# Kernel optimization log

Measured on AMD Instinct MI355X. Metric: run time of the kernel, lower is better.

The kernel has to match this reference:

```python
import jax, jax.numpy as jnp
import numpy as np

N, HID, EDGE_DIM, E = 512, 16, 8, 8192
H4 = HID * 4


def _mlp(x, params):
    W0, b0, W1, b1, W2, b2, W3, b3 = params
    h = jax.nn.relu(x @ W0 + b0)
    h = jax.nn.relu(h @ W1 + b1)
    h = jax.nn.relu(h @ W2 + b2)
    return h @ W3 + b3


def setup_inputs() -> dict:
    key = jax.random.key(0)
    ks = jax.random.split(key, 16)
    rng = np.random.default_rng(0)
    flat = rng.choice(N * N, size=E, replace=False)  # unique edges -> add == set
    edge_index = jnp.asarray(np.stack([flat // N, flat % N]), dtype=jnp.int32)

    def lin(k, fan_in, fan_out):
        kw, kb = jax.random.split(k)
        s = 1.0 / np.sqrt(fan_in)
        return (jax.random.uniform(kw, (fan_in, fan_out), jnp.float32, -s, s),
                jax.random.uniform(kb, (fan_out,), jnp.float32, -s, s))

    W0, b0 = lin(ks[0], EDGE_DIM, H4)
    W1, b1 = lin(ks[1], H4, H4)
    W2, b2 = lin(ks[2], H4, H4)
    W3, b3 = lin(ks[3], H4, HID * HID)
    V0, c0 = lin(ks[4], HID, H4)
    V1, c1 = lin(ks[5], H4, H4)
    V2, c2 = lin(ks[6], H4, H4)
    V3, c3 = lin(ks[7], H4, HID)
    L, Lb = lin(ks[8], HID, HID)

    return {
        'mtr': jax.random.normal(ks[9], (N, N, HID), jnp.float32),
        'edge_attr': jax.random.normal(ks[10], (E, EDGE_DIM), jnp.float32),
        'edge_index': edge_index,
        'W0': W0, 'b0': b0, 'W1': W1, 'b1': b1, 'W2': W2, 'b2': b2, 'W3': W3, 'b3': b3,
        'V0': V0, 'c0': c0, 'V1': V1, 'c1': c1, 'V2': V2, 'c2': c2, 'V3': V3, 'c3': c3,
        'L': L, 'Lb': Lb,
    }


def reference(mtr, edge_attr, edge_index,
              W0, b0, W1, b1, W2, b2, W3, b3,
              V0, c0, V1, c1, V2, c2, V3, c3,
              L, Lb):
    n, hid = mtr.shape[0], mtr.shape[2]
    src, dst = edge_index[0], edge_index[1]
    # per-edge hid x hid matrices (edge_fc)
    F = _mlp(edge_attr, (W0, b0, W1, b1, W2, b2, W3, b3)).reshape(-1, hid, hid)
    # sparse form of einsum('ijc,jkct->ikt', mtr, fmtr): gather src column,
    # per-edge matmul, scatter-add into dst column (edges unique -> == dense set)
    msg = jnp.einsum('iec,ect->iet', mtr[:, src, :], F)          # [n, E, hid]
    mtr1 = jax.ops.segment_sum(msg.transpose(1, 0, 2), dst, num_segments=n)  # [k, i, t]
    mtr1 = mtr1.transpose(1, 0, 2)                                # [i, k, t]
    idx = jnp.arange(n)
    mtr1 = mtr1.at[idx, idx, :].set(0.0)
    mtr1 = mtr1 / hid
    trans = mtr1.transpose(1, 0, 2) @ L + Lb                      # linear(mtr1^T)
    return mtr + _mlp(mtr1 + trans, (V0, c0, V1, c1, V2, c2, V3, c3))
```

## Files before the change

### kernel.cpp

```cpp
#include <hip/hip_runtime.h>
#include <hip/hip_bf16.h>

#define NN 512
#define EE 8192

#define OFF_F     0u
#define OFF_MTR1  2097152u
#define OFF_W     6291456u
#define WR_W0   0
#define WR_B0   512
#define WR_W1   576
#define WR_B1   4672
#define WR_W2   4736
#define WR_B2   8832
#define WR_W3   8896
#define WR_B3   25280
#define WR_V0T  25536
#define WR_C0   26560
#define WR_V1   26624
#define WR_C1   30720
#define WR_V2   30784
#define WR_C2   34880
#define WR_V3   34944
#define WR_C3   35968
#define WR_L    35984
#define WR_LB   36240
#define W_TOTAL 36256
#define OFF_OFFS    (OFF_W + W_TOTAL)
#define OFF_SORTED  (OFF_OFFS + 513)
#define OFF_FLAG    (OFF_SORTED + EE)
#define OFF_MTRT    6336420u
#define OFF_OFFSP   8433572u
#define OFF_PACKP   8434085u
#define OFF_FPACK   8442792u
#define OFF_VPACK   9491496u
#define WS_NEED_BYTES  ((size_t)(OFF_MTRT  + 2097152u) * 4u)
#define WS_FULL2_BYTES ((size_t)(OFF_VPACK + 5632u) * 4u)

#define VP0OFF 0
#define VP1OFF 2048
#define VP2OFF 6144
#define VP3OFF 10240

#define XSTR 72
#define RSTR 20

typedef __attribute__((ext_vector_type(8))) short bf16x8;
typedef __attribute__((ext_vector_type(4))) float f32x4;

__device__ __forceinline__ float bflo(unsigned u){ return __uint_as_float(u << 16); }
__device__ __forceinline__ float bfhi(unsigned u){ return __uint_as_float(u & 0xffff0000u); }
__device__ __forceinline__ unsigned short f2bf(float f){
  __hip_bfloat16 h = __float2bfloat16(f);
  union { __hip_bfloat16 hh; unsigned short ss; } u;
  u.hh = h; return u.ss;
}
__device__ __forceinline__ unsigned pack2(float a, float b){
  return (unsigned)f2bf(a) | ((unsigned)f2bf(b) << 16);
}
__device__ __forceinline__ float cvt(float v){ return v; }
__device__ __forceinline__ float cvt(__hip_bfloat16 v){ return __bfloat162float(v); }

__device__ __forceinline__ void load16f(const void* base, size_t eoff, int f32, float m[16]) {
  if (f32) {
    const float4* p = (const float4*)((const float*)base + eoff);
    float4 a = p[0], b = p[1], c = p[2], d = p[3];
    m[0]=a.x; m[1]=a.y; m[2]=a.z; m[3]=a.w;
    m[4]=b.x; m[5]=b.y; m[6]=b.z; m[7]=b.w;
    m[8]=c.x; m[9]=c.y; m[10]=c.z; m[11]=c.w;
    m[12]=d.x; m[13]=d.y; m[14]=d.z; m[15]=d.w;
  } else {
    const uint4* p = (const uint4*)((const __hip_bfloat16*)base + eoff);
    uint4 u0 = p[0], u1 = p[1];
    m[0]=bflo(u0.x);  m[1]=bfhi(u0.x);  m[2]=bflo(u0.y);  m[3]=bfhi(u0.y);
    m[4]=bflo(u0.z);  m[5]=bfhi(u0.z);  m[6]=bflo(u0.w);  m[7]=bfhi(u0.w);
    m[8]=bflo(u1.x);  m[9]=bfhi(u1.x);  m[10]=bflo(u1.y); m[11]=bfhi(u1.y);
    m[12]=bflo(u1.z); m[13]=bfhi(u1.z); m[14]=bflo(u1.w); m[15]=bfhi(u1.w);
  }
}

__device__ __forceinline__ float ldelem(const void* p, int idx, int f32) {
  return f32 ? ((const float*)p)[idx]
             : __bfloat162float(((const __hip_bfloat16*)p)[idx]);
}

__device__ __forceinline__ int detect_f32_local(const unsigned short* mtr_u16, float* red) {
  int tid = threadIdx.x;
  float m = 0.f;
  for (int t = tid; t < 4096; t += 512) {
    float v = __uint_as_float(((unsigned)mtr_u16[t]) << 16);
    if (v != v) m = 3e38f;
    else m = fmaxf(m, fabsf(v));
  }
  red[tid] = m;
  __syncthreads();
  for (int s = 256; s > 0; s >>= 1) {
    if (tid < s) red[tid] = fmaxf(red[tid], red[tid + s]);
    __syncthreads();
  }
  float mx = red[0];
  __syncthreads();
  return (mx > 1e6f) ? 1 : 0;
}

template <typename T>
__device__ void edge_body(const T* __restrict__ ea,
                          const T* __restrict__ W0, const T* __restrict__ b0,
                          const T* __restrict__ W1, const T* __restrict__ b1,
                          const T* __restrict__ W2, const T* __restrict__ b2,
                          const T* __restrict__ W3, const T* __restrict__ b3,
                          int e, int eg, int lane,
                          float (*shA)[64], float (*shB)[64],
                          unsigned short* __restrict__ Fpack)
{
  float x[8];
  #pragma unroll
  for (int c = 0; c < 8; c++) x[c] = cvt(ea[(size_t)e * 8 + c]);

  float s = cvt(b0[lane]);
  #pragma unroll
  for (int c = 0; c < 8; c++) s += x[c] * cvt(W0[c * 64 + lane]);
  shA[eg][lane] = fmaxf(s, 0.f);
  __syncthreads();

  s = cvt(b1[lane]);
  #pragma unroll
  for (int c = 0; c < 64; c++) s += shA[eg][c] * cvt(W1[c * 64 + lane]);
  shB[eg][lane] = fmaxf(s, 0.f);
  __syncthreads();

  s = cvt(b2[lane]);
  #pragma unroll
  for (int c = 0; c < 64; c++) s += shB[eg][c] * cvt(W2[c * 64 + lane]);
  shA[eg][lane] = fmaxf(s, 0.f);
  __syncthreads();

  int quad = lane >> 4, tt = lane & 15;
  #pragma unroll
  for (int r = 0; r < 4; r++) {
    int o = r * 64 + lane;
    float t = cvt(b3[o]);
    #pragma unroll
    for (int c = 0; c < 64; c++) t += shA[eg][c] * cvt(W3[c * 256 + o]);
    int cc = r * 4 + quad;
    Fpack[(size_t)e * 256 + (cc >> 3) * 128 + tt * 8 + (cc & 7)] = f2bf(t);
  }
}

__global__ __launch_bounds__(512) void prep_all(
  const void* __restrict__ mtr, const void* __restrict__ ea, const int* __restrict__ ei,
  const void* __restrict__ W0, const void* __restrict__ b0,
  const void* __restrict__ W1, const void* __restrict__ b1,
  const void* __restrict__ W2, const void* __restrict__ b2,
  const void* __restrict__ W3, const void* __restrict__ b3,
  const void* __restrict__ V0, const void* __restrict__ c0,
  const void* __restrict__ V1, const void* __restrict__ c1,
  const void* __restrict__ V2, const void* __restrict__ c2,
  const void* __restrict__ V3, const void* __restrict__ c3,
  const void* __restrict__ L,  const void* __restrict__ Lb,
  int* __restrict__ flag, float* __restrict__ w, unsigned short* __restrict__ VP,
  int* __restrict__ offsP, unsigned* __restrict__ packP,
  unsigned short* __restrict__ Fpack, __hip_bfloat16* __restrict__ mtrT)
{
  __shared__ __attribute__((aligned(16))) char smem_raw[8192];
  int tid = threadIdx.x;
  int bid = blockIdx.x;
  const int f32 = detect_f32_local((const unsigned short*)mtr, (float*)smem_raw);

  if (bid == 0) {
    int* cnt  = (int*)smem_raw;
    int* pcs  = cnt + 512;
    int* curP = pcs + 512;
    cnt[tid] = 0;
    if (tid == 0) flag[0] = f32;
    __syncthreads();
    for (int e = tid; e < EE; e += 512) atomicAdd(&cnt[ei[EE + e]], 1);
    __syncthreads();
    int myc = cnt[tid];
    int myp = (myc + 1) & ~1;
    pcs[tid] = myp;
    __syncthreads();
    for (int off = 1; off < 512; off <<= 1) {
      int b = (tid >= off) ? pcs[tid - off] : 0;
      __syncthreads();
      pcs[tid] += b;
      __syncthreads();
    }
    int excP = pcs[tid] - myp;
    offsP[tid] = excP;
    if (tid == 511) offsP[512] = pcs[511];
    curP[tid] = excP;
    if (myc & 1) packP[excP + myc] = EE;
    __syncthreads();
    for (int e = tid; e < EE; e += 512) {
      int d = ei[EE + e];
      int s = ei[e];
      packP[atomicAdd(&curP[d], 1)] = (unsigned)e | ((unsigned)s << 14);
    }
    unsigned* fz = (unsigned*)(Fpack + (size_t)EE * 256);
    for (int i2 = tid; i2 < 128; i2 += 512) fz[i2] = 0u;
  } else if (bid < 33) {
    int g = (bid - 1) * 512 + tid;
    const int stride = 32 * 512;
    auto cv = [&](const void* p, int off, int n){
      for (int i = g; i < n; i += stride) w[off + i] = ldelem(p, i, f32);
    };
    cv(W0, WR_W0, 512);  cv(b0, WR_B0, 64);
    cv(W1, WR_W1, 4096); cv(b1, WR_B1, 64);
    cv(W2, WR_W2, 4096); cv(b2, WR_B2, 64);
    cv(W3, WR_W3, 16384);cv(b3, WR_B3, 256);
    for (int idx = g; idx < 1024; idx += stride) {
      int j = idx >> 4, t = idx & 15;
      w[WR_V0T + idx] = ldelem(V0, t * 64 + j, f32);
    }
    cv(c0, WR_C0, 64);
    cv(V1, WR_V1, 4096); cv(c1, WR_C1, 64);
    cv(V2, WR_V2, 4096); cv(c2, WR_C2, 64);
    cv(V3, WR_V3, 1024); cv(c3, WR_C3, 16);
    cv(L,  WR_L,  256);  cv(Lb, WR_LB, 16);
  } else if (bid < 37) {
    int g = (bid - 33) * 512 + tid;
    const int stride = 4 * 512;
    for (int idx = g; idx < 2048; idx += stride) {
      int j = idx & 7, lp = (idx >> 3) & 63, nt = idx >> 9;
      int nn = lp & 15, qq = lp >> 4;
      int kk = qq * 8 + j;
      float v = (kk < 16) ? ldelem(V0, kk * 64 + nt * 16 + nn, f32) : 0.f;
      VP[VP0OFF + idx] = f2bf(v);
    }
    for (int idx = g; idx < 4096; idx += stride) {
      int j = idx & 7, lp = (idx >> 3) & 63, tile = idx >> 9;
      int nn = lp & 15, qq = lp >> 4;
      int kc = tile >> 2, nt = tile & 3;
      int kk = kc * 32 + qq * 8 + j;
      VP[VP1OFF + idx] = f2bf(ldelem(V1, kk * 64 + nt * 16 + nn, f32));
      VP[VP2OFF + idx] = f2bf(ldelem(V2, kk * 64 + nt * 16 + nn, f32));
    }
    for (int idx = g; idx < 1024; idx += stride) {
      int j = idx & 7, lp = (idx >> 3) & 63, kc = idx >> 9;
      int nn = lp & 15, qq = lp >> 4;
      int kk = kc * 32 + qq * 8 + j;
      VP[VP3OFF + idx] = f2bf(ldelem(V3, kk * 16 + nn, f32));
    }
  } else if (bid < 549) {
    int s = bid - 37;
    int i = tid;
    float m[16];
    load16f(mtr, (size_t)i * 8192 + (size_t)s * 16, f32, m);
    unsigned pw[8];
    #pragma unroll
    for (int q = 0; q < 8; q++) pw[q] = pack2(m[2*q], m[2*q+1]);
    uint4* op = (uint4*)(mtrT + (size_t)s * 8192 + (size_t)i * 16);
    op[0] = make_uint4(pw[0], pw[1], pw[2], pw[3]);
    op[1] = make_uint4(pw[4], pw[5], pw[6], pw[7]);
  } else {
    int eg = tid >> 6, lane = tid & 63;
    int e = (bid - 549) * 8 + eg;
    float (*shA)[64] = (float(*)[64])smem_raw;
    float (*shB)[64] = (float(*)[64])(smem_raw + 2048);
    if (f32)
      edge_body<float>((const float*)ea,
        (const float*)W0, (const float*)b0, (const float*)W1, (const float*)b1,
        (const float*)W2, (const float*)b2, (const float*)W3, (const float*)b3,
        e, eg, lane, shA, shB, Fpack);
    else
      edge_body<__hip_bfloat16>((const __hip_bfloat16*)ea,
        (const __hip_bfloat16*)W0, (const __hip_bfloat16*)b0,
        (const __hip_bfloat16*)W1, (const __hip_bfloat16*)b1,
        (const __hip_bfloat16*)W2, (const __hip_bfloat16*)b2,
        (const __hip_bfloat16*)W3, (const __hip_bfloat16*)b3,
        e, eg, lane, shA, shB, Fpack);
  }
}

__global__ __launch_bounds__(256) void message_mfma2(
  const __hip_bfloat16* __restrict__ mtrT,
  const unsigned short* __restrict__ Fpack,
  const int* __restrict__ offsP, const unsigned* __restrict__ packP,
  float* __restrict__ mtr1T)
{
  int k = blockIdx.x;
  int tid = threadIdx.x;
  int wave = tid >> 6, lane = tid & 63;
  int n = lane & 15, quad = lane >> 4;
  int qh = quad >> 1, qq = quad & 1;
  int ibase = blockIdx.y * 256 + wave * 64;
  int j0 = offsP[k], j1 = offsP[k + 1];

  f32x4 acc[4];
  #pragma unroll
  for (int mt = 0; mt < 4; mt++) acc[mt] = (f32x4){0.f, 0.f, 0.f, 0.f};

  bf16x8 bfrag;
  bf16x8 af0, af1, af2, af3;
  auto loadfr = [&](int j) {
    unsigned p1 = __builtin_amdgcn_readfirstlane(packP[j]);
    unsigned p2 = __builtin_amdgcn_readfirstlane(packP[j + 1]);
    unsigned pv = qh ? p2 : p1;
    int es = (int)(pv & 0x3FFFu);
    int ss = (int)(pv >> 14);
    bfrag = *(const bf16x8*)(Fpack + (size_t)es * 256 + (qq * 16 + n) * 8);
    const __hip_bfloat16* ab = mtrT + (size_t)ss * 8192 + qq * 8;
    af0 = *(const bf16x8*)(ab + (size_t)(ibase + 0 * 16 + n) * 16);
    af1 = *(const bf16x8*)(ab + (size_t)(ibase + 1 * 16 + n) * 16);
    af2 = *(const bf16x8*)(ab + (size_t)(ibase + 2 * 16 + n) * 16);
    af3 = *(const bf16x8*)(ab + (size_t)(ibase + 3 * 16 + n) * 16);
  };
  if (j0 < j1) loadfr(j0);
  for (int j = j0; j < j1; j += 2) {
    bf16x8 bc = bfrag, a0 = af0, a1 = af1, a2 = af2, a3 = af3;
    if (j + 2 < j1) loadfr(j + 2);
    acc[0] = __builtin_amdgcn_mfma_f32_16x16x32_bf16(a0, bc, acc[0], 0, 0, 0);
    acc[1] = __builtin_amdgcn_mfma_f32_16x16x32_bf16(a1, bc, acc[1], 0, 0, 0);
    acc[2] = __builtin_amdgcn_mfma_f32_16x16x32_bf16(a2, bc, acc[2], 0, 0, 0);
    acc[3] = __builtin_amdgcn_mfma_f32_16x16x32_bf16(a3, bc, acc[3], 0, 0, 0);
  }

  float* obase = mtr1T + (size_t)k * 8192;
  #pragma unroll
  for (int mt = 0; mt < 4; mt++) {
    int irow = ibase + mt * 16 + quad * 4;
    #pragma unroll
    for (int reg = 0; reg < 4; reg++)
      obase[(size_t)(irow + reg) * 16 + n] = acc[mt][reg];
  }
}

__global__ __launch_bounds__(256, 4) void final_mfma(
  const void* __restrict__ mtr, const float* __restrict__ w,
  const float* __restrict__ mtr1T, const int* __restrict__ flag,
  const unsigned short* __restrict__ VP, void* __restrict__ out)
{
  const int f32 = flag[0];
  __shared__ __attribute__((aligned(16))) unsigned short XB[256 * XSTR];
  int tid = threadIdx.x;
  int ti = blockIdx.x >> 5, tk = blockIdx.x & 31;
  int r = tid >> 4, c = tid & 15;
  int i = ti * 16 + r, k = tk * 16 + c;
  float scale = (i == k) ? 0.f : 0.0625f;

  float y[16];
  {
    float a[16], b[16];
    const float4* pa = (const float4*)(mtr1T + (size_t)k * 8192 + (size_t)i * 16);
    const float4* pb = (const float4*)(mtr1T + (size_t)i * 8192 + (size_t)k * 16);
    #pragma unroll
    for (int q4 = 0; q4 < 4; q4++) {
      float4 va = pa[q4], vb = pb[q4];
      a[q4*4+0]=va.x*scale; a[q4*4+1]=va.y*scale; a[q4*4+2]=va.z*scale; a[q4*4+3]=va.w*scale;
      b[q4*4+0]=vb.x*scale; b[q4*4+1]=vb.y*scale; b[q4*4+2]=vb.z*scale; b[q4*4+3]=vb.w*scale;
    }
    const float* Lf  = w + WR_L;
    const float* Lbf = w + WR_LB;
    #pragma unroll
    for (int t = 0; t < 16; t++) y[t] = a[t] + Lbf[t];
    #pragma unroll
    for (int cc = 0; cc < 16; cc++) {
      #pragma unroll
      for (int t = 0; t < 16; t++) y[t] += b[cc] * Lf[cc * 16 + t];
    }
  }
  {
    uint4* row = (uint4*)(XB + tid * XSTR);
    row[0] = make_uint4(pack2(y[0],y[1]),  pack2(y[2],y[3]),
                        pack2(y[4],y[5]),  pack2(y[6],y[7]));
    row[1] = make_uint4(pack2(y[8],y[9]),  pack2(y[10],y[11]),
                        pack2(y[12],y[13]),pack2(y[14],y[15]));
    row[2] = make_uint4(0,0,0,0);
    row[3] = make_uint4(0,0,0,0);
  }

  int wave = tid >> 6, lane = tid & 63;
  int m15 = lane & 15, q = lane >> 4;
  int mtb = wave * 4;

  {
    bf16x8 af[4];
    #pragma unroll
    for (int t4 = 0; t4 < 4; t4++)
      af[t4] = *(const bf16x8*)(XB + ((mtb + t4) * 16 + m15) * XSTR + q * 8);
    #pragma unroll
    for (int nt = 0; nt < 4; nt++) {
      bf16x8 bf_ = *(const bf16x8*)(VP + VP0OFF + nt * 512 + (q * 16 + m15) * 8);
      float bias = w[WR_C0 + nt * 16 + m15];
      #pragma unroll
      for (int t4 = 0; t4 < 4; t4++) {
        f32x4 acc = (f32x4){0.f,0.f,0.f,0.f};
        acc = __builtin_amdgcn_mfma_f32_16x16x32_bf16(af[t4], bf_, acc, 0, 0, 0);
        int pbase = (mtb + t4) * 16 + q * 4;
        #pragma unroll
        for (int reg = 0; reg < 4; reg++)
          XB[(pbase + reg) * XSTR + nt * 16 + m15] = f2bf(fmaxf(acc[reg] + bias, 0.f));
      }
    }
  }
  #pragma unroll
  for (int layer = 0; layer < 2; layer++) {
    int vpo  = layer ? VP2OFF : VP1OFF;
    int wrc  = layer ? WR_C2  : WR_C1;
    bf16x8 af[8];
    #pragma unroll
    for (int t4 = 0; t4 < 4; t4++) {
      #pragma unroll
      for (int kc = 0; kc < 2; kc++)
        af[t4*2+kc] = *(const bf16x8*)(XB + ((mtb + t4) * 16 + m15) * XSTR + kc * 32 + q * 8);
    }
    #pragma unroll
    for (int nt = 0; nt < 4; nt++) {
      bf16x8 b0 = *(const bf16x8*)(VP + vpo + (0 * 4 + nt) * 512 + (q * 16 + m15) * 8);
      bf16x8 b1 = *(const bf16x8*)(VP + vpo + (1 * 4 + nt) * 512 + (q * 16 + m15) * 8);
      float bias = w[wrc + nt * 16 + m15];
      #pragma unroll
      for (int t4 = 0; t4 < 4; t4++) {
        f32x4 acc = (f32x4){0.f,0.f,0.f,0.f};
        acc = __builtin_amdgcn_mfma_f32_16x16x32_bf16(af[t4*2+0], b0, acc, 0, 0, 0);
        acc = __builtin_amdgcn_mfma_f32_16x16x32_bf16(af[t4*2+1], b1, acc, 0, 0, 0);
        int pbase = (mtb + t4) * 16 + q * 4;
        #pragma unroll
        for (int reg = 0; reg < 4; reg++)
          XB[(pbase + reg) * XSTR + nt * 16 + m15] = f2bf(fmaxf(acc[reg] + bias, 0.f));
      }
    }
  }
  f32x4 acc4[4];
  float bias4;
  {
    bf16x8 af[8];
    #pragma unroll
    for (int t4 = 0; t4 < 4; t4++) {
      #pragma unroll
      for (int kc = 0; kc < 2; kc++)
        af[t4*2+kc] = *(const bf16x8*)(XB + ((mtb + t4) * 16 + m15) * XSTR + kc * 32 + q * 8);
    }
    bf16x8 b0 = *(const bf16x8*)(VP + VP3OFF + 0 * 512 + (q * 16 + m15) * 8);
    bf16x8 b1 = *(const bf16x8*)(VP + VP3OFF + 1 * 512 + (q * 16 + m15) * 8);
    bias4 = w[WR_C3 + m15];
    #pragma unroll
    for (int t4 = 0; t4 < 4; t4++) {
      f32x4 acc = (f32x4){0.f,0.f,0.f,0.f};
      acc = __builtin_amdgcn_mfma_f32_16x16x32_bf16(af[t4*2+0], b0, acc, 0, 0, 0);
      acc = __builtin_amdgcn_mfma_f32_16x16x32_bf16(af[t4*2+1], b1, acc, 0, 0, 0);
      acc4[t4] = acc;
    }
  }
  __syncthreads();
  float* RRB = (float*)XB;
  #pragma unroll
  for (int t4 = 0; t4 < 4; t4++) {
    int pbase = (mtb + t4) * 16 + q * 4;
    #pragma unroll
    for (int reg = 0; reg < 4; reg++)
      RRB[(pbase + reg) * RSTR + m15] = acc4[t4][reg] + bias4;
  }
  float rr[16];
  {
    const float4* rp = (const float4*)(RRB + tid * RSTR);
    float4 v0 = rp[0], v1 = rp[1], v2 = rp[2], v3 = rp[3];
    rr[0]=v0.x; rr[1]=v0.y; rr[2]=v0.z; rr[3]=v0.w;
    rr[4]=v1.x; rr[5]=v1.y; rr[6]=v1.z; rr[7]=v1.w;
    rr[8]=v2.x; rr[9]=v2.y; rr[10]=v2.z; rr[11]=v2.w;
    rr[12]=v3.x; rr[13]=v3.y; rr[14]=v3.z; rr[15]=v3.w;
  }
  size_t base = (size_t)i * 8192 + (size_t)k * 16;
  float mv[16];
  load16f(mtr, base, f32, mv);
  if (f32) {
    float4* op = (float4*)((float*)out + base);
    op[0] = make_float4(mv[0]+rr[0],  mv[1]+rr[1],  mv[2]+rr[2],  mv[3]+rr[3]);
    op[1] = make_float4(mv[4]+rr[4],  mv[5]+rr[5],  mv[6]+rr[6],  mv[7]+rr[7]);
    op[2] = make_float4(mv[8]+rr[8],  mv[9]+rr[9],  mv[10]+rr[10],mv[11]+rr[11]);
    op[3] = make_float4(mv[12]+rr[12],mv[13]+rr[13],mv[14]+rr[14],mv[15]+rr[15]);
  } else {
    unsigned pw[8];
    #pragma unroll
    for (int q2 = 0; q2 < 8; q2++)
      pw[q2] = pack2(mv[2*q2] + rr[2*q2], mv[2*q2+1] + rr[2*q2+1]);
    uint4* op = (uint4*)((__hip_bfloat16*)out + base);
    op[0] = make_uint4(pw[0], pw[1], pw[2], pw[3]);
    op[1] = make_uint4(pw[4], pw[5], pw[6], pw[7]);
  }
}

__global__ void prep_weights(
  const void* __restrict__ W0, const void* __restrict__ b0,
  const void* __restrict__ W1, const void* __restrict__ b1,
  const void* __restrict__ W2, const void* __restrict__ b2,
  const void* __restrict__ W3, const void* __restrict__ b3,
  const void* __restrict__ V0, const void* __restrict__ c0,
  const void* __restrict__ V1, const void* __restrict__ c1,
  const void* __restrict__ V2, const void* __restrict__ c2,
  const void* __restrict__ V3, const void* __restrict__ c3,
  const void* __restrict__ L,  const void* __restrict__ Lb,
  const unsigned short* __restrict__ mtr_u16,
  int* __restrict__ flag, float* __restrict__ w)
{
  __shared__ float mx[256];
  int tid = threadIdx.x;
  float m = 0.f;
  for (int t = tid; t < 4096; t += 256) {
    float v = __uint_as_float(((unsigned)mtr_u16[t]) << 16);
    if (v != v) m = 3e38f;
    else m = fmaxf(m, fabsf(v));
  }
  mx[tid] = m;
  __syncthreads();
  for (int s = 128; s > 0; s >>= 1) {
    if (tid < s) mx[tid] = fmaxf(mx[tid], mx[tid + s]);
    __syncthreads();
  }
  const int f32 = (mx[0] > 1e6f) ? 1 : 0;
  if (blockIdx.x == 0 && tid == 0) flag[0] = f32;

  int g = blockIdx.x * blockDim.x + tid;
  int stride = gridDim.x * blockDim.x;
  auto cv = [&](const void* p, int off, int n){
    for (int i = g; i < n; i += stride) w[off + i] = ldelem(p, i, f32);
  };
  cv(W0, WR_W0, 512);  cv(b0, WR_B0, 64);
  cv(W1, WR_W1, 4096); cv(b1, WR_B1, 64);
  cv(W2, WR_W2, 4096); cv(b2, WR_B2, 64);
  cv(W3, WR_W3, 16384);cv(b3, WR_B3, 256);
  for (int idx = g; idx < 1024; idx += stride) {
    int j = idx >> 4, t = idx & 15;
    w[WR_V0T + idx] = ldelem(V0, t * 64 + j, f32);
  }
  cv(c0, WR_C0, 64);
  cv(V1, WR_V1, 4096); cv(c1, WR_C1, 64);
  cv(V2, WR_V2, 4096); cv(c2, WR_C2, 64);
  cv(V3, WR_V3, 1024); cv(c3, WR_C3, 16);
  cv(L,  WR_L,  256);  cv(Lb, WR_LB, 16);
}

__global__ void build_bins_basic(const int* __restrict__ ei,
                                 int* __restrict__ offs, int* __restrict__ sorted)
{
  __shared__ int cnt[512];
  __shared__ int cur[512];
  int tid = threadIdx.x;
  cnt[tid] = 0;
  __syncthreads();
  for (int e = tid; e < EE; e += 512) atomicAdd(&cnt[ei[EE + e]], 1);
  __syncthreads();
  int myc = cnt[tid];
  for (int off = 1; off < 512; off <<= 1) {
    int add = (tid >= off) ? cnt[tid - off] : 0;
    __syncthreads();
    cnt[tid] += add;
    __syncthreads();
  }
  int excl = cnt[tid] - myc;
  offs[tid] = excl;
  if (tid == 511) offs[512] = cnt[511];
  cur[tid] = excl;
  __syncthreads();
  for (int e = tid; e < EE; e += 512) {
    int d = ei[EE + e];
    sorted[atomicAdd(&cur[d], 1)] = e;
  }
}

__global__ __launch_bounds__(256) void edge_mlp_fb(
  const void* __restrict__ ea, const float* __restrict__ w,
  const int* __restrict__ flag, float* __restrict__ Fws)
{
  const int f32 = flag[0];
  const float* W0f = w + WR_W0; const float* b0f = w + WR_B0;
  const float* W1f = w + WR_W1; const float* b1f = w + WR_B1;
  const float* W2f = w + WR_W2; const float* b2f = w + WR_B2;
  const float* W3f = w + WR_W3; const float* b3f = w + WR_B3;
  int tid = threadIdx.x;
  int eg = tid >> 6, lane = tid & 63;
  int e = blockIdx.x * 4 + eg;
  __shared__ float shA[4][64];
  __shared__ float shB[4][64];
  float x[8];
  #pragma unroll
  for (int c = 0; c < 8; c++) x[c] = ldelem(ea, e * 8 + c, f32);
  float s = b0f[lane];
  #pragma unroll
  for (int c = 0; c < 8; c++) s += x[c] * W0f[c * 64 + lane];
  shA[eg][lane] = fmaxf(s, 0.f);
  __syncthreads();
  s = b1f[lane];
  #pragma unroll
  for (int c = 0; c < 64; c++) s += shA[eg][c] * W1f[c * 64 + lane];
  shB[eg][lane] = fmaxf(s, 0.f);
  __syncthreads();
  s = b2f[lane];
  #pragma unroll
  for (int c = 0; c < 64; c++) s += shB[eg][c] * W2f[c * 64 + lane];
  shA[eg][lane] = fmaxf(s, 0.f);
  __syncthreads();
  #pragma unroll
  for (int r2 = 0; r2 < 4; r2++) {
    int o = r2 * 64 + lane;
    float t = b3f[o];
    #pragma unroll
    for (int c = 0; c < 64; c++) t += shA[eg][c] * W3f[c * 256 + o];
    Fws[(size_t)e * 256 + o] = t;
  }
}

__global__ __launch_bounds__(256) void message_kernel_direct(
  const void* __restrict__ mtr, const int* __restrict__ ei,
  const float* __restrict__ Fws, const int* __restrict__ offs,
  const int* __restrict__ sorted, const int* __restrict__ flag,
  float* __restrict__ mtr1T)
{
  const int f32 = flag[0];
  int k = blockIdx.x;
  int i = blockIdx.y * 256 + threadIdx.x;
  float acc[16];
  #pragma unroll
  for (int t = 0; t < 16; t++) acc[t] = 0.f;
  int j0 = offs[k], j1 = offs[k + 1];
  for (int j = j0; j < j1; j++) {
    int e = __builtin_amdgcn_readfirstlane(sorted[j]);
    int s = __builtin_amdgcn_readfirstlane(ei[e]);
    float m[16];
    load16f(mtr, (size_t)i * 8192 + s * 16, f32, m);
    const float4* Fe = (const float4*)(Fws + (size_t)e * 256);
    #pragma unroll
    for (int c = 0; c < 16; c++) {
      float4 f0 = Fe[c*4+0], f1 = Fe[c*4+1], f2 = Fe[c*4+2], f3 = Fe[c*4+3];
      acc[0]  += m[c]*f0.x; acc[1]  += m[c]*f0.y; acc[2]  += m[c]*f0.z; acc[3]  += m[c]*f0.w;
      acc[4]  += m[c]*f1.x; acc[5]  += m[c]*f1.y; acc[6]  += m[c]*f1.z; acc[7]  += m[c]*f1.w;
      acc[8]  += m[c]*f2.x; acc[9]  += m[c]*f2.y; acc[10] += m[c]*f2.z; acc[11] += m[c]*f2.w;
      acc[12] += m[c]*f3.x; acc[13] += m[c]*f3.y; acc[14] += m[c]*f3.z; acc[15] += m[c]*f3.w;
    }
  }
  float4* op = (float4*)(mtr1T + (size_t)k * 8192 + i * 16);
  op[0] = make_float4(acc[0],  acc[1],  acc[2],  acc[3]);
  op[1] = make_float4(acc[4],  acc[5],  acc[6],  acc[7]);
  op[2] = make_float4(acc[8],  acc[9],  acc[10], acc[11]);
  op[3] = make_float4(acc[12], acc[13], acc[14], acc[15]);
}

__global__ __launch_bounds__(256, 4) void final_kernel_fb(
  const void* __restrict__ mtr, const float* __restrict__ w,
  const float* __restrict__ mtr1T, const int* __restrict__ flag,
  void* __restrict__ out)
{
  const int f32 = flag[0];
  __shared__ unsigned hbuf[32 * 256];
  int tid = threadIdx.x;
  int ti = blockIdx.x >> 5, tk = blockIdx.x & 31;
  int r = tid >> 4, c = tid & 15;
  int i = ti * 16 + r, k = tk * 16 + c;
  float scale = (i == k) ? 0.f : 0.0625f;
  float y[16];
  {
    float a[16], b[16];
    const float4* pa = (const float4*)(mtr1T + (size_t)k * 8192 + (size_t)i * 16);
    const float4* pb = (const float4*)(mtr1T + (size_t)i * 8192 + (size_t)k * 16);
    #pragma unroll
    for (int q = 0; q < 4; q++) {
      float4 va = pa[q], vb = pb[q];
      a[q*4+0]=va.x*scale; a[q*4+1]=va.y*scale; a[q*4+2]=va.z*scale; a[q*4+3]=va.w*scale;
      b[q*4+0]=vb.x*scale; b[q*4+1]=vb.y*scale; b[q*4+2]=vb.z*scale; b[q*4+3]=vb.w*scale;
    }
    const float* Lf  = w + WR_L;
    const float* Lbf = w + WR_LB;
    #pragma unroll
    for (int t = 0; t < 16; t++) y[t] = a[t] + Lbf[t];
    #pragma unroll
    for (int cc = 0; cc < 16; cc++) {
      #pragma unroll
      for (int t = 0; t < 16; t++) y[t] += b[cc] * Lf[cc * 16 + t];
    }
  }
  {
    const float* V0t = w + WR_V0T; const float* c0f = w + WR_C0;
    for (int m = 0; m < 32; m++) {
      float s0 = c0f[2*m], s1 = c0f[2*m+1];
      #pragma unroll
      for (int t = 0; t < 16; t++) {
        s0 += y[t] * V0t[(2*m) * 16 + t];
        s1 += y[t] * V0t[(2*m+1) * 16 + t];
      }
      hbuf[m * 256 + tid] = pack2(fmaxf(s0, 0.f), fmaxf(s1, 0.f));
    }
  }
  #pragma unroll
  for (int lyr = 0; lyr < 2; lyr++) {
    const float* Vf = w + (lyr ? WR_V2 : WR_V1);
    const float* cf = w + (lyr ? WR_C2 : WR_C1);
    unsigned held[16];
    #pragma unroll
    for (int pass = 0; pass < 2; pass++) {
      float s[32];
      #pragma unroll
      for (int jj = 0; jj < 32; jj++) s[jj] = cf[pass * 32 + jj];
      for (int m = 0; m < 32; m++) {
        unsigned hu = hbuf[m * 256 + tid];
        float h0 = bflo(hu), h1 = bfhi(hu);
        #pragma unroll
        for (int jj = 0; jj < 32; jj++)
          s[jj] += h0 * Vf[(2*m) * 64 + pass*32 + jj] + h1 * Vf[(2*m+1) * 64 + pass*32 + jj];
      }
      if (pass == 0) {
        #pragma unroll
        for (int q = 0; q < 16; q++) held[q] = pack2(fmaxf(s[2*q], 0.f), fmaxf(s[2*q+1], 0.f));
      } else {
        #pragma unroll
        for (int q = 0; q < 16; q++) hbuf[q * 256 + tid] = held[q];
        #pragma unroll
        for (int q = 0; q < 16; q++) hbuf[(16 + q) * 256 + tid] = pack2(fmaxf(s[2*q], 0.f), fmaxf(s[2*q+1], 0.f));
      }
    }
  }
  float rr[16];
  {
    const float* V3f = w + WR_V3; const float* c3f = w + WR_C3;
    #pragma unroll
    for (int t = 0; t < 16; t++) rr[t] = c3f[t];
    for (int m = 0; m < 32; m++) {
      unsigned hu = hbuf[m * 256 + tid];
      float h0 = bflo(hu), h1 = bfhi(hu);
      #pragma unroll
      for (int t = 0; t < 16; t++)
        rr[t] += h0 * V3f[(2*m) * 16 + t] + h1 * V3f[(2*m+1) * 16 + t];
    }
  }
  size_t base = (size_t)i * 8192 + (size_t)k * 16;
  float mv[16];
  load16f(mtr, base, f32, mv);
  if (f32) {
    float4* op = (float4*)((float*)out + base);
    op[0] = make_float4(mv[0]+rr[0],  mv[1]+rr[1],  mv[2]+rr[2],  mv[3]+rr[3]);
    op[1] = make_float4(mv[4]+rr[4],  mv[5]+rr[5],  mv[6]+rr[6],  mv[7]+rr[7]);
    op[2] = make_float4(mv[8]+rr[8],  mv[9]+rr[9],  mv[10]+rr[10],mv[11]+rr[11]);
    op[3] = make_float4(mv[12]+rr[12],mv[13]+rr[13],mv[14]+rr[14],mv[15]+rr[15]);
  } else {
    unsigned pw[8];
    #pragma unroll
    for (int q = 0; q < 8; q++)
      pw[q] = pack2(mv[2*q] + rr[2*q], mv[2*q+1] + rr[2*q+1]);
    uint4* op = (uint4*)((__hip_bfloat16*)out + base);
    op[0] = make_uint4(pw[0], pw[1], pw[2], pw[3]);
    op[1] = make_uint4(pw[4], pw[5], pw[6], pw[7]);
  }
}

extern "C" void kernel_launch(void* const* d_in, const int* in_sizes, int n_in,
                              void* d_out, int out_size, void* d_ws, size_t ws_size,
                              hipStream_t stream)
{
  const void* mtr = d_in[0];
  const void* ea  = d_in[1];
  const int*  ei  = (const int*)d_in[2];

  float* ws    = (float*)d_ws;
  float* Fws   = ws + OFF_F;
  float* mtr1T = ws + OFF_MTR1;
  float* w     = ws + OFF_W;
  int* offs    = (int*)(ws + OFF_OFFS);
  int* sorted  = (int*)(ws + OFF_SORTED);
  int* flag    = (int*)(ws + OFF_FLAG);
  __hip_bfloat16* mtrT = (__hip_bfloat16*)(ws + OFF_MTRT);
  int* offsP   = (int*)(ws + OFF_OFFSP);
  unsigned* packP = (unsigned*)(ws + OFF_PACKP);
  unsigned short* Fpack = (unsigned short*)(ws + OFF_FPACK);
  unsigned short* VP    = (unsigned short*)(ws + OFF_VPACK);

  if (ws_size >= WS_FULL2_BYTES) {
    prep_all<<<1573, 512, 0, stream>>>(
        mtr, ea, ei,
        d_in[3], d_in[4], d_in[5], d_in[6], d_in[7], d_in[8], d_in[9], d_in[10],
        d_in[11], d_in[12], d_in[13], d_in[14], d_in[15], d_in[16], d_in[17], d_in[18],
        d_in[19], d_in[20],
        flag, w, VP, offsP, packP, Fpack, mtrT);
    dim3 gmsg(512, 2);
    message_mfma2<<<gmsg, 256, 0, stream>>>(mtrT, Fpack, offsP, packP, mtr1T);
    final_mfma<<<1024, 256, 0, stream>>>(mtr, w, mtr1T, flag, VP, d_out);
  } else {
    prep_weights<<<32, 256, 0, stream>>>(d_in[3], d_in[4], d_in[5], d_in[6],
                                         d_in[7], d_in[8], d_in[9], d_in[10],
                                         d_in[11], d_in[12], d_in[13], d_in[14],
                                         d_in[15], d_in[16], d_in[17], d_in[18],
                                         d_in[19], d_in[20],
                                         (const unsigned short*)mtr, flag, w);
    build_bins_basic<<<1, 512, 0, stream>>>(ei, offs, sorted);
    edge_mlp_fb<<<EE / 4, 256, 0, stream>>>(ea, w, flag, Fws);
    dim3 gmsg(512, 2);
    message_kernel_direct<<<gmsg, 256, 0, stream>>>(mtr, ei, Fws, offs, sorted, flag, mtr1T);
    final_kernel_fb<<<1024, 256, 0, stream>>>(mtr, w, mtr1T, flag, d_out);
  }
}
```

Before: 192.1 us.

## Store mtr1 as bf16, split message grid finer, swizzle final LDS layout

The message kernel now writes its intermediate in bf16 instead of fp32 and uses a 512x4 grid with two tiles per wave, which doubles the number of blocks. The final kernel stages both mtr1 tiles into LDS with coalesced loads. It also replaces the padded activation rows with an unpadded, XOR-swizzled layout and raises the occupancy hint to 5 blocks. The intent is to halve intermediate traffic, improve coalescing and cut LDS use and bank conflicts. The cost is bf16 rounding of the aggregated messages and an extra __syncthreads in the final kernel.

```diff
diff --git a/kernel.cpp b/kernel.cpp
--- a/kernel.cpp
+++ b/kernel.cpp
@@ -42,7 +42,7 @@
 #define VP2OFF 6144
 #define VP3OFF 10240
 
-#define XSTR 72
+#define XS   64
 #define RSTR 20
 
 typedef __attribute__((ext_vector_type(8))) short bf16x8;
@@ -277,22 +277,20 @@
   const __hip_bfloat16* __restrict__ mtrT,
   const unsigned short* __restrict__ Fpack,
   const int* __restrict__ offsP, const unsigned* __restrict__ packP,
-  float* __restrict__ mtr1T)
+  __hip_bfloat16* __restrict__ mtr1B)
 {
   int k = blockIdx.x;
   int tid = threadIdx.x;
   int wave = tid >> 6, lane = tid & 63;
   int n = lane & 15, quad = lane >> 4;
   int qh = quad >> 1, qq = quad & 1;
-  int ibase = blockIdx.y * 256 + wave * 64;
+  int ibase = blockIdx.y * 128 + wave * 32;
   int j0 = offsP[k], j1 = offsP[k + 1];
 
-  f32x4 acc[4];
-  #pragma unroll
-  for (int mt = 0; mt < 4; mt++) acc[mt] = (f32x4){0.f, 0.f, 0.f, 0.f};
-
-  bf16x8 bfrag;
-  bf16x8 af0, af1, af2, af3;
+  f32x4 acc0 = (f32x4){0.f,0.f,0.f,0.f};
+  f32x4 acc1 = (f32x4){0.f,0.f,0.f,0.f};
+
+  bf16x8 bfrag, af0, af1;
   auto loadfr = [&](int j) {
     unsigned p1 = __builtin_amdgcn_readfirstlane(packP[j]);
     unsigned p2 = __builtin_amdgcn_readfirstlane(packP[j + 1]);
@@ -303,71 +301,92 @@
     const __hip_bfloat16* ab = mtrT + (size_t)ss * 8192 + qq * 8;
     af0 = *(const bf16x8*)(ab + (size_t)(ibase + 0 * 16 + n) * 16);
     af1 = *(const bf16x8*)(ab + (size_t)(ibase + 1 * 16 + n) * 16);
-    af2 = *(const bf16x8*)(ab + (size_t)(ibase + 2 * 16 + n) * 16);
-    af3 = *(const bf16x8*)(ab + (size_t)(ibase + 3 * 16 + n) * 16);
   };
   if (j0 < j1) loadfr(j0);
   for (int j = j0; j < j1; j += 2) {
-    bf16x8 bc = bfrag, a0 = af0, a1 = af1, a2 = af2, a3 = af3;
+    bf16x8 bc = bfrag, a0 = af0, a1 = af1;
     if (j + 2 < j1) loadfr(j + 2);
-    acc[0] = __builtin_amdgcn_mfma_f32_16x16x32_bf16(a0, bc, acc[0], 0, 0, 0);
-    acc[1] = __builtin_amdgcn_mfma_f32_16x16x32_bf16(a1, bc, acc[1], 0, 0, 0);
-    acc[2] = __builtin_amdgcn_mfma_f32_16x16x32_bf16(a2, bc, acc[2], 0, 0, 0);
-    acc[3] = __builtin_amdgcn_mfma_f32_16x16x32_bf16(a3, bc, acc[3], 0, 0, 0);
-  }
-
-  float* obase = mtr1T + (size_t)k * 8192;
-  #pragma unroll
-  for (int mt = 0; mt < 4; mt++) {
-    int irow = ibase + mt * 16 + quad * 4;
-    #pragma unroll
-    for (int reg = 0; reg < 4; reg++)
-      obase[(size_t)(irow + reg) * 16 + n] = acc[mt][reg];
-  }
-}
-
-__global__ __launch_bounds__(256, 4) void final_mfma(
+    acc0 = __builtin_amdgcn_mfma_f32_16x16x32_bf16(a0, bc, acc0, 0, 0, 0);
+    acc1 = __builtin_amdgcn_mfma_f32_16x16x32_bf16(a1, bc, acc1, 0, 0, 0);
+  }
+
+  __hip_bfloat16* obase = mtr1B + (size_t)k * 8192;
+  #pragma unroll
+  for (int reg = 0; reg < 4; reg++) {
+    int r0 = ibase + 0 * 16 + quad * 4 + reg;
+    int r1 = ibase + 1 * 16 + quad * 4 + reg;
+    obase[(size_t)r0 * 16 + n] = __float2bfloat16(acc0[reg]);
+    obase[(size_t)r1 * 16 + n] = __float2bfloat16(acc1[reg]);
+  }
+}
+
+__global__ __launch_bounds__(256, 5) void final_mfma(
   const void* __restrict__ mtr, const float* __restrict__ w,
-  const float* __restrict__ mtr1T, const int* __restrict__ flag,
+  const __hip_bfloat16* __restrict__ mtr1B, const int* __restrict__ flag,
   const unsigned short* __restrict__ VP, void* __restrict__ out)
 {
   const int f32 = flag[0];
-  __shared__ __attribute__((aligned(16))) unsigned short XB[256 * XSTR];
+  __shared__ __attribute__((aligned(16))) unsigned short XB[256 * XS];
   int tid = threadIdx.x;
   int ti = blockIdx.x >> 5, tk = blockIdx.x & 31;
+  int i0 = ti * 16, k0 = tk * 16;
+
+  {
+    int row = tid >> 4, off = tid & 15;
+    const uint4* ga = (const uint4*)(mtr1B + (size_t)(k0 + row) * 8192 + (size_t)i0 * 16);
+    const uint4* gb = (const uint4*)(mtr1B + (size_t)(i0 + row) * 8192 + (size_t)k0 * 16);
+    uint4* la = (uint4*)(XB + row * 264);
+    uint4* lb = (uint4*)(XB + 4224 + row * 264);
+    la[off*2]   = ga[off*2];
+    la[off*2+1] = ga[off*2+1];
+    lb[off*2]   = gb[off*2];
+    lb[off*2+1] = gb[off*2+1];
+  }
+  __syncthreads();
+
   int r = tid >> 4, c = tid & 15;
-  int i = ti * 16 + r, k = tk * 16 + c;
+  int i = i0 + r, k = k0 + c;
   float scale = (i == k) ? 0.f : 0.0625f;
 
   float y[16];
   {
-    float a[16], b[16];
-    const float4* pa = (const float4*)(mtr1T + (size_t)k * 8192 + (size_t)i * 16);
-    const float4* pb = (const float4*)(mtr1T + (size_t)i * 8192 + (size_t)k * 16);
-    #pragma unroll
-    for (int q4 = 0; q4 < 4; q4++) {
-      float4 va = pa[q4], vb = pb[q4];
-      a[q4*4+0]=va.x*scale; a[q4*4+1]=va.y*scale; a[q4*4+2]=va.z*scale; a[q4*4+3]=va.w*scale;
-      b[q4*4+0]=vb.x*scale; b[q4*4+1]=vb.y*scale; b[q4*4+2]=vb.z*scale; b[q4*4+3]=vb.w*scale;
-    }
+    const uint4* ap = (const uint4*)(XB + c * 264 + r * 16);
+    const uint4* bp = (const uint4*)(XB + 4224 + r * 264 + c * 16);
+    uint4 a0 = ap[0], a1 = ap[1], b0 = bp[0], b1 = bp[1];
+    float a_[16], b_[16];
+    a_[0]=bflo(a0.x);  a_[1]=bfhi(a0.x);  a_[2]=bflo(a0.y);  a_[3]=bfhi(a0.y);
+    a_[4]=bflo(a0.z);  a_[5]=bfhi(a0.z);  a_[6]=bflo(a0.w);  a_[7]=bfhi(a0.w);
+    a_[8]=bflo(a1.x);  a_[9]=bfhi(a1.x);  a_[10]=bflo(a1.y); a_[11]=bfhi(a1.y);
+    a_[12]=bflo(a1.z); a_[13]=bfhi(a1.z); a_[14]=bflo(a1.w); a_[15]=bfhi(a1.w);
+    b_[0]=bflo(b0.x);  b_[1]=bfhi(b0.x);  b_[2]=bflo(b0.y);  b_[3]=bfhi(b0.y);
+    b_[4]=bflo(b0.z);  b_[5]=bfhi(b0.z);  b_[6]=bflo(b0.w);  b_[7]=bfhi(b0.w);
+    b_[8]=bflo(b1.x);  b_[9]=bfhi(b1.x);  b_[10]=bflo(b1.y); b_[11]=bfhi(b1.y);
+    b_[12]=bflo(b1.z); b_[13]=bfhi(b1.z); b_[14]=bflo(b1.w); b_[15]=bfhi(b1.w);
     const float* Lf  = w + WR_L;
     const float* Lbf = w + WR_LB;
     #pragma unroll
-    for (int t = 0; t < 16; t++) y[t] = a[t] + Lbf[t];
+    for (int t = 0; t < 16; t++) y[t] = a_[t] * scale + Lbf[t];
     #pragma unroll
     for (int cc = 0; cc < 16; cc++) {
+      float bs = b_[cc] * scale;
       #pragma unroll
-      for (int t = 0; t < 16; t++) y[t] += b[cc] * Lf[cc * 16 + t];
-    }
-  }
+      for (int t = 0; t < 16; t++) y[t] += bs * Lf[cc * 16 + t];
+    }
+  }
+  __syncthreads();
+
   {
-    uint4* row = (uint4*)(XB + tid * XSTR);
-    row[0] = make_uint4(pack2(y[0],y[1]),  pack2(y[2],y[3]),
-                        pack2(y[4],y[5]),  pack2(y[6],y[7]));
-    row[1] = make_uint4(pack2(y[8],y[9]),  pack2(y[10],y[11]),
-                        pack2(y[12],y[13]),pack2(y[14],y[15]));
-    row[2] = make_uint4(0,0,0,0);
-    row[3] = make_uint4(0,0,0,0);
+    unsigned sw = tid & 7;
+    uint4 d0 = make_uint4(pack2(y[0],y[1]),  pack2(y[2],y[3]),
+                          pack2(y[4],y[5]),  pack2(y[6],y[7]));
+    uint4 d1 = make_uint4(pack2(y[8],y[9]),  pack2(y[10],y[11]),
+                          pack2(y[12],y[13]),pack2(y[14],y[15]));
+    uint4 z = make_uint4(0,0,0,0);
+    uint4* rowp = (uint4*)(XB + tid * XS);
+    rowp[0 ^ sw] = d0;
+    rowp[1 ^ sw] = d1;
+    rowp[2 ^ sw] = z;
+    rowp[3 ^ sw] = z;
   }
 
   int wave = tid >> 6, lane = tid & 63;
@@ -377,20 +396,25 @@
   {
     bf16x8 af[4];
     #pragma unroll
-    for (int t4 = 0; t4 < 4; t4++)
-      af[t4] = *(const bf16x8*)(XB + ((mtb + t4) * 16 + m15) * XSTR + q * 8);
+    for (int t4 = 0; t4 < 4; t4++) {
+      int row = (mtb + t4) * 16 + m15;
+      af[t4] = *(const bf16x8*)(XB + row * XS + ((q ^ (row & 7)) * 8));
+    }
     #pragma unroll
     for (int nt = 0; nt < 4; nt++) {
       bf16x8 bf_ = *(const bf16x8*)(VP + VP0OFF + nt * 512 + (q * 16 + m15) * 8);
       float bias = w[WR_C0 + nt * 16 + m15];
+      int g = nt * 2 + (m15 >> 3), off = m15 & 7;
       #pragma unroll
       for (int t4 = 0; t4 < 4; t4++) {
         f32x4 acc = (f32x4){0.f,0.f,0.f,0.f};
         acc = __builtin_amdgcn_mfma_f32_16x16x32_bf16(af[t4], bf_, acc, 0, 0, 0);
         int pbase = (mtb + t4) * 16 + q * 4;
         #pragma unroll
-        for (int reg = 0; reg < 4; reg++)
-          XB[(pbase + reg) * XSTR + nt * 16 + m15] = f2bf(fmaxf(acc[reg] + bias, 0.f));
+        for (int reg = 0; reg < 4; reg++) {
+          int row = pbase + reg;
+          XB[row * XS + ((g ^ (row & 7)) * 8 + off)] = f2bf(fmaxf(acc[reg] + bias, 0.f));
+        }
       }
     }
   }
@@ -401,15 +425,17 @@
     bf16x8 af[8];
     #pragma unroll
     for (int t4 = 0; t4 < 4; t4++) {
+      int row = (mtb + t4) * 16 + m15;
       #pragma unroll
       for (int kc = 0; kc < 2; kc++)
-        af[t4*2+kc] = *(const bf16x8*)(XB + ((mtb + t4) * 16 + m15) * XSTR + kc * 32 + q * 8);
+        af[t4*2+kc] = *(const bf16x8*)(XB + row * XS + (((kc*4 + q) ^ (row & 7)) * 8));
     }
     #pragma unroll
     for (int nt = 0; nt < 4; nt++) {
       bf16x8 b0 = *(const bf16x8*)(VP + vpo + (0 * 4 + nt) * 512 + (q * 16 + m15) * 8);
       bf16x8 b1 = *(const bf16x8*)(VP + vpo + (1 * 4 + nt) * 512 + (q * 16 + m15) * 8);
       float bias = w[wrc + nt * 16 + m15];
+      int g = nt * 2 + (m15 >> 3), off = m15 & 7;
       #pragma unroll
       for (int t4 = 0; t4 < 4; t4++) {
         f32x4 acc = (f32x4){0.f,0.f,0.f,0.f};
@@ -417,8 +443,10 @@
         acc = __builtin_amdgcn_mfma_f32_16x16x32_bf16(af[t4*2+1], b1, acc, 0, 0, 0);
         int pbase = (mtb + t4) * 16 + q * 4;
         #pragma unroll
-        for (int reg = 0; reg < 4; reg++)
-          XB[(pbase + reg) * XSTR + nt * 16 + m15] = f2bf(fmaxf(acc[reg] + bias, 0.f));
+        for (int reg = 0; reg < 4; reg++) {
+          int row = pbase + reg;
+          XB[row * XS + ((g ^ (row & 7)) * 8 + off)] = f2bf(fmaxf(acc[reg] + bias, 0.f));
+        }
       }
     }
   }
@@ -428,9 +456,10 @@
     bf16x8 af[8];
     #pragma unroll
     for (int t4 = 0; t4 < 4; t4++) {
+      int row = (mtb + t4) * 16 + m15;
       #pragma unroll
       for (int kc = 0; kc < 2; kc++)
-        af[t4*2+kc] = *(const bf16x8*)(XB + ((mtb + t4) * 16 + m15) * XSTR + kc * 32 + q * 8);
+        af[t4*2+kc] = *(const bf16x8*)(XB + row * XS + (((kc*4 + q) ^ (row & 7)) * 8));
     }
     bf16x8 b0 = *(const bf16x8*)(VP + VP3OFF + 0 * 512 + (q * 16 + m15) * 8);
     bf16x8 b1 = *(const bf16x8*)(VP + VP3OFF + 1 * 512 + (q * 16 + m15) * 8);
@@ -753,6 +782,7 @@
   float* ws    = (float*)d_ws;
   float* Fws   = ws + OFF_F;
   float* mtr1T = ws + OFF_MTR1;
+  __hip_bfloat16* mtr1B = (__hip_bfloat16*)(ws + OFF_MTR1);
   float* w     = ws + OFF_W;
   int* offs    = (int*)(ws + OFF_OFFS);
   int* sorted  = (int*)(ws + OFF_SORTED);
@@ -770,9 +800,9 @@
         d_in[11], d_in[12], d_in[13], d_in[14], d_in[15], d_in[16], d_in[17], d_in[18],
         d_in[19], d_in[20],
         flag, w, VP, offsP, packP, Fpack, mtrT);
-    dim3 gmsg(512, 2);
-    message_mfma2<<<gmsg, 256, 0, stream>>>(mtrT, Fpack, offsP, packP, mtr1T);
-    final_mfma<<<1024, 256, 0, stream>>>(mtr, w, mtr1T, flag, VP, d_out);
+    dim3 gmsg(512, 4);
+    message_mfma2<<<gmsg, 256, 0, stream>>>(mtrT, Fpack, offsP, packP, mtr1B);
+    final_mfma<<<1024, 256, 0, stream>>>(mtr, w, mtr1B, flag, VP, d_out);
   } else {
     prep_weights<<<32, 256, 0, stream>>>(d_in[3], d_in[4], d_in[5], d_in[6],
                                          d_in[7], d_in[8], d_in[9], d_in[10],
```

After: 214.2 us. +11.5%, slower.
